# Optimization experiments

Measured on AMD Instinct MI355X. Metric: run time of the kernel, lower is better.

The kernel has to match this reference:

```python
import jax, jax.numpy as jnp
import numpy as np

B, L, E, H, D, DFF = 2, 2048, 1024, 16, 64, 4096
SCALE = D ** 0.5


def rmsnorm(x):
    # NOTE: original uses mean(x*x)**0.5 with no eps and no learned scale
    rms = jnp.sqrt(jnp.mean(x * x, axis=-1, keepdims=True))
    return x / rms


def alibi_matrix():
    i = jnp.arange(L)
    dists = -jnp.abs(i[None, :] - i[:, None]).astype(jnp.float32)  # [L, L]
    slopes = 2.0 ** (-jnp.linspace(1.0, 8.0, H))                   # [H]
    alibi = slopes[:, None, None] * dists                          # [H, L, L]
    causal = jnp.tril(jnp.ones((L, L), dtype=bool))
    return jnp.where(causal[None], alibi, -jnp.inf)[None]          # [1, H, L, L]


def setup_inputs() -> dict:
    key = jax.random.key(0)
    ks = jax.random.split(key, 16)
    s = 0.02
    return {
        "X": jax.random.normal(ks[0], (B, L, E), jnp.float32),
        "encoder_out": jax.random.normal(ks[1], (B, L, E), jnp.float32),
        # self-attention params
        "Wqkv": jax.random.normal(ks[2], (E, 3 * H * D), jnp.float32) * s,
        "bqkv": jnp.zeros((3 * H * D,), jnp.float32),
        "Wo_sa": jax.random.normal(ks[3], (H * D, E), jnp.float32) * s,
        "bo_sa": jnp.zeros((E,), jnp.float32),
        # cross-attention params (computed by torch module but its forward returns X, so unused)
        "Wq": jax.random.normal(ks[4], (E, H * D), jnp.float32) * s,
        "bq": jnp.zeros((H * D,), jnp.float32),
        "Wkv": jax.random.normal(ks[5], (E, 2 * H * D), jnp.float32) * s,
        "bkv": jnp.zeros((2 * H * D,), jnp.float32),
        "Wo_ca": jax.random.normal(ks[6], (H * D, E), jnp.float32) * s,
        "bo_ca": jnp.zeros((E,), jnp.float32),
        # GLU FFN params (bias=False)
        "Ww": jax.random.normal(ks[7], (E, DFF), jnp.float32) * s,
        "Wv": jax.random.normal(ks[8], (E, DFF), jnp.float32) * s,
        "Wout": jax.random.normal(ks[9], (DFF, E), jnp.float32) * s,
    }


def reference(X, encoder_out, Wqkv, bqkv, Wo_sa, bo_sa, Wq, bq, Wkv, bkv,
              Wo_ca, bo_ca, Ww, Wv, Wout):
    alibi = alibi_matrix()

    # ---- self-attention (pre-norm + residual) ----
    h = rmsnorm(X)
    qkv = (h @ Wqkv + bqkv).reshape(B, L, H, 3, D)
    Q, K, V = qkv[..., 0, :], qkv[..., 1, :], qkv[..., 2, :]      # [B, L, H, D]
    scores = jnp.einsum('blhd,bmhd->bhlm', Q, K) / SCALE + alibi  # [B, H, L, L]
    attn = jax.nn.softmax(scores, axis=-1)
    ctx = jnp.einsum('bhlm,bmhd->blhd', attn, V).reshape(B, L, H * D)
    X = X + ctx @ Wo_sa + bo_sa

    # ---- cross-attention stage ----
    # Faithful to source: CrossAttention.forward returns its input X (the
    # normalized tensor) rather than the attention output, so this block is
    # X + rmsnorm(X). Cross-attn params never affect the output.
    X = X + rmsnorm(X)

    # ---- GLU FFN (pre-norm + residual), exact (erf) GELU as in torch F.gelu ----
    h = rmsnorm(X)
    ff = jax.nn.gelu(h @ Ww, approximate=False) * (h @ Wv)
    X = X + ff @ Wout
    return X
```

## Files before the change

### kernel.cpp

```cpp
#include <hip/hip_runtime.h>

#define B_SZ 2
#define L_SEQ 2048
#define E_DIM 1024
#define NH 16
#define DH 64
#define DFF_DIM 4096
#define ROWS (B_SZ * L_SEQ)
#define NCID 80

typedef __attribute__((ext_vector_type(8))) short short8;
typedef __attribute__((ext_vector_type(4))) float f32x4;

__device__ __forceinline__ short f2bf(float f) {
  unsigned u = __builtin_bit_cast(unsigned, f);
  u = (u + 0x7FFFu + ((u >> 16) & 1u)) >> 16;
  return (short)u;
}
__device__ __forceinline__ float bf2f(short s) {
  unsigned u = ((unsigned)(unsigned short)s) << 16;
  return __builtin_bit_cast(float, u);
}
__device__ __forceinline__ unsigned pack2bf(float lo, float hi) {
  return ((unsigned)(unsigned short)f2bf(hi) << 16) |
         (unsigned)(unsigned short)f2bf(lo);
}

__device__ __forceinline__ float fast_gelu(float x) {
  float ax = fabsf(x) * 0.70710678118654752f;
  float t = __builtin_amdgcn_rcpf(__builtin_fmaf(0.3275911f, ax, 1.0f));
  float p = t * __builtin_fmaf(
                    t,
                    __builtin_fmaf(
                        t,
                        __builtin_fmaf(t,
                                       __builtin_fmaf(t, 1.061405429f,
                                                      -1.453152027f),
                                       1.421413741f),
                        -0.284496736f),
                    0.254829592f);
  float erf = 1.0f - p * __expf(-ax * ax);
  erf = copysignf(erf, x);
  return 0.5f * x * (1.0f + erf);
}

__device__ __forceinline__ void async_copy16(const void* g, void* l) {
  __builtin_amdgcn_global_load_lds(
      (const __attribute__((address_space(1))) void*)g,
      (__attribute__((address_space(3))) void*)l, 16, 0, 0);
}

__device__ __forceinline__ float block_sum256(float v) {
  __shared__ float sbuf[4];
#pragma unroll
  for (int off = 32; off > 0; off >>= 1) v += __shfl_xor(v, off, 64);
  int lane = threadIdx.x & 63, w = threadIdx.x >> 6;
  if (lane == 0) sbuf[w] = v;
  __syncthreads();
  return sbuf[0] + sbuf[1] + sbuf[2] + sbuf[3];
}

__global__ __launch_bounds__(256) void prep_all(
    const float* __restrict__ Wqkv, const float* __restrict__ Wo,
    const float* __restrict__ Ww, const float* __restrict__ Wv,
    const float* __restrict__ Wout, const float* __restrict__ X,
    short* __restrict__ Bqkv3, short* __restrict__ WoT,
    short* __restrict__ Bcat, short* __restrict__ WoutT,
    short* __restrict__ H) {
  __shared__ float tile[32][33];
  int b = blockIdx.x;
  if (b < 16384) {
    const float* W;
    short* Wt;
    int K, N, mode, bx, by;
    if (b < 3072) {
      W = Wqkv; Wt = Bqkv3; K = 1024; N = 3072; mode = 1;
      bx = b % 96; by = b / 96;
    } else if (b < 4096) {
      int c = b - 3072;
      W = Wo; Wt = WoT; K = 1024; N = 1024; mode = 1;
      bx = c & 31; by = c >> 5;
    } else if (b < 8192) {
      int c = b - 4096;
      W = Ww; Wt = Bcat; K = 1024; N = 4096; mode = 2;
      bx = c & 127; by = c >> 7;
    } else if (b < 12288) {
      int c = b - 8192;
      W = Wv; Wt = Bcat; K = 1024; N = 4096; mode = 3;
      bx = c & 127; by = c >> 7;
    } else {
      int c = b - 12288;
      W = Wout; Wt = WoutT; K = 4096; N = 1024; mode = 1;
      bx = c & 31; by = c >> 5;
    }
    int n0 = bx * 32, k0 = by * 32;
    int tx = threadIdx.x & 31, ty = threadIdx.x >> 5;
#pragma unroll
    for (int i = 0; i < 4; i++)
      tile[ty + 8 * i][tx] = W[(size_t)(k0 + ty + 8 * i) * N + n0 + tx];
    __syncthreads();
#pragma unroll
    for (int i = 0; i < 4; i++) {
      int n = n0 + ty + 8 * i;
      int orow = (mode == 1)
                     ? n
                     : ((n >> 5) * 64 + (n & 31) + (mode == 3 ? 32 : 0));
      Wt[(size_t)orow * K + k0 + tx] = f2bf(tile[tx][ty + 8 * i]);
    }
  } else {
    size_t row = b - 16384;
    float4 v = ((const float4*)(X + row * E_DIM))[threadIdx.x];
    float ss = v.x * v.x + v.y * v.y + v.z * v.z + v.w * v.w;
    ss = block_sum256(ss);
    float inv = rsqrtf(ss * (1.0f / E_DIM));
    short* h = H + row * E_DIM + (size_t)threadIdx.x * 4;
    h[0] = f2bf(v.x * inv);
    h[1] = f2bf(v.y * inv);
    h[2] = f2bf(v.z * inv);
    h[3] = f2bf(v.w * inv);
  }
}

__global__ __launch_bounds__(256) void resid_rms_fused(
    const float* __restrict__ X, const float* __restrict__ P0,
    const float* __restrict__ P1, const float* __restrict__ bias,
    float* __restrict__ Xout, short* __restrict__ H) {
  size_t row = blockIdx.x;
  int t = threadIdx.x;
  float4 v = ((const float4*)(X + row * E_DIM))[t];
  float4 a = ((const float4*)(P0 + row * E_DIM))[t];
  float4 b = ((const float4*)(P1 + row * E_DIM))[t];
  float4 c = ((const float4*)bias)[t];
  v.x += a.x + b.x + c.x;
  v.y += a.y + b.y + c.y;
  v.z += a.z + b.z + c.z;
  v.w += a.w + b.w + c.w;
  float ss = v.x * v.x + v.y * v.y + v.z * v.z + v.w * v.w;
  ss = block_sum256(ss);
  float inv = rsqrtf(ss * (1.0f / E_DIM));
  float4 o;
  o.x = v.x * (1.0f + inv);
  o.y = v.y * (1.0f + inv);
  o.z = v.z * (1.0f + inv);
  o.w = v.w * (1.0f + inv);
  ((float4*)(Xout + row * E_DIM))[t] = o;
  short* h = H + row * E_DIM + (size_t)t * 4;
  h[0] = f2bf(v.x * inv);
  h[1] = f2bf(v.y * inv);
  h[2] = f2bf(v.z * inv);
  h[3] = f2bf(v.w * inv);
}

__global__ __launch_bounds__(256) void add2_k(const float* __restrict__ P0,
                                              const float* __restrict__ P1,
                                              float* __restrict__ out) {
  size_t i = (size_t)blockIdx.x * 256 + threadIdx.x;
  float4 v = ((const float4*)out)[i];
  float4 a = ((const float4*)P0)[i];
  float4 b = ((const float4*)P1)[i];
  v.x += a.x + b.x;
  v.y += a.y + b.y;
  v.z += a.z + b.z;
  v.w += a.w + b.w;
  ((float4*)out)[i] = v;
}

__global__ __launch_bounds__(256, 2) void gemm_bt(
    const short* __restrict__ A, const short* __restrict__ Bt,
    const float* __restrict__ bias, void* __restrict__ out,
    void* __restrict__ out2, void* __restrict__ out3, int M, int N, int K,
    int epi, int ksplit) {
  __shared__ short smem[128 * 32 * 4];
  short* As0 = smem;
  short* Bs0 = smem + 4096;
  short* As1 = smem + 8192;
  short* Bs1 = smem + 12288;
  int t = threadIdx.x;
  int lane = t & 63;
  int quad = lane >> 4, l16 = lane & 15;
  int wave = t >> 6;
  int wr = wave >> 1, wc = wave & 1;
  int m0 = blockIdx.y * 128, n0 = blockIdx.x * 128;
  int klen = K / ksplit;
  int kstart = blockIdx.z * klen;

  f32x4 acc[4][4];
#pragma unroll
  for (int i = 0; i < 4; i++)
#pragma unroll
    for (int j = 0; j < 4; j++) acc[i][j] = (f32x4){0.f, 0.f, 0.f, 0.f};

  for (int k0 = kstart; k0 < kstart + klen; k0 += 64) {
    __syncthreads();
#pragma unroll
    for (int p = 0; p < 2; p++) {
      int s = p * 256 + t;
      int mm = s >> 2, kk = (s & 3) * 8;
      const short* ag = A + (size_t)(m0 + mm) * K + k0 + kk;
      const short* bg = Bt + (size_t)(n0 + mm) * K + k0 + kk;
      async_copy16(ag, As0 + (size_t)s * 8);
      async_copy16(bg, Bs0 + (size_t)s * 8);
      async_copy16(ag + 32, As1 + (size_t)s * 8);
      async_copy16(bg + 32, Bs1 + (size_t)s * 8);
    }
    __syncthreads();
#pragma unroll
    for (int half = 0; half < 2; half++) {
      const short* As = half ? As1 : As0;
      const short* Bs = half ? Bs1 : Bs0;
      short8 af[4], bfv[4];
#pragma unroll
      for (int i = 0; i < 4; i++) {
        af[i] = *(const short8*)&As[(wr * 64 + i * 16 + l16) * 32 + quad * 8];
        bfv[i] = *(const short8*)&Bs[(wc * 64 + i * 16 + l16) * 32 + quad * 8];
      }
#pragma unroll
      for (int mi = 0; mi < 4; mi++)
#pragma unroll
        for (int ni = 0; ni < 4; ni++)
          acc[mi][ni] = __builtin_amdgcn_mfma_f32_16x16x32_bf16(
              af[mi], bfv[ni], acc[mi][ni], 0, 0, 0);
    }
  }

  if (epi == 5) {
    short* FF = (short*)out;
    int ffbase = blockIdx.x * 64 + wc * 32;
#pragma unroll
    for (int mi = 0; mi < 4; mi++)
#pragma unroll
      for (int ni = 0; ni < 2; ni++)
#pragma unroll
        for (int r = 0; r < 4; r++) {
          int rowl = wr * 64 + mi * 16 + quad * 4 + r;
          float g = fast_gelu(acc[mi][ni][r]);
          FF[(size_t)(m0 + rowl) * DFF_DIM + ffbase + ni * 16 + l16] =
              f2bf(g * acc[mi][ni + 2][r]);
        }
    return;
  }

#pragma unroll
  for (int mi = 0; mi < 4; mi++) {
#pragma unroll
    for (int ni = 0; ni < 4; ni++) {
      int col = n0 + wc * 64 + ni * 16 + l16;
#pragma unroll
      for (int r = 0; r < 4; r++) {
        int row = m0 + wr * 64 + mi * 16 + quad * 4 + r;
        float v = acc[mi][ni][r];
        if (epi == 4) {
          float* po = (float*)out + (size_t)blockIdx.z * ((size_t)M * N);
          po[(size_t)row * N + col] = v;
        } else {
          v += bias[col];
          int h = col / 192;
          int rem = col - h * 192;
          int ty = rem >> 6, d = rem & 63;
          short* dst = (ty == 0) ? (short*)out
                                 : ((ty == 1) ? (short*)out2 : (short*)out3);
          int bb = row >> 11, l = row & 2047;
          dst[((size_t)(bb * NH + h) * L_SEQ + l) * DH + d] = f2bf(v);
        }
      }
    }
  }
}

__global__ __launch_bounds__(512, 2) void gemm256(
    const short* __restrict__ A, const short* __restrict__ Bt,
    const float* __restrict__ bias, void* __restrict__ out,
    void* __restrict__ out2, void* __restrict__ out3, int M, int N, int K,
    int epi) {
  __shared__ __align__(16) short smem[65536];
  (void)M;
  (void)N;
  int t = threadIdx.x;
  int lane = t & 63;
  int quad = lane >> 4, l16 = lane & 15;
  int wave = t >> 6;
  int wr = wave >> 2;
  int wc = wave & 3;
  int m0 = blockIdx.y * 256, n0 = blockIdx.x * 256;

  int row0 = t >> 3;
  int sl = (t & 7) ^ (row0 & 7);
  int goff = row0 * K + sl * 8;
  int ldw = t * 16;
  char* smc = (char*)smem;
  auto stageHT = [&](const short* gsrc, int ldsbase) {
    async_copy16(gsrc + goff, smc + ldsbase + ldw);
    async_copy16(gsrc + goff + (K << 6), smc + ldsbase + 8192 + ldw);
  };

  int swz = (l16 & 7) << 4;
  int colp0 = (quad * 16) ^ swz;
  int colp1 = (64 + quad * 16) ^ swz;
  const char* aB = smc + wr * 16384 + l16 * 128;
  const char* bB = smc + 32768 + (wc >> 1) * 16384 + (wc & 1) * 8192 +
                   l16 * 128;

  f32x4 acc[8][4];
#pragma unroll
  for (int i = 0; i < 8; i++)
#pragma unroll
    for (int j = 0; j < 4; j++) acc[i][j] = (f32x4){0.f, 0.f, 0.f, 0.f};
  short8 areg[4][2], breg[4][2];

  const short* Am0 = A + (size_t)m0 * K;
  const short* Am1 = A + (size_t)(m0 + 128) * K;
  const short* Bn0 = Bt + (size_t)n0 * K;
  const short* Bn1 = Bt + (size_t)(n0 + 128) * K;

  stageHT(Am0, 0);
  stageHT(Am1, 16384);
  stageHT(Bn0, 32768);
  stageHT(Bn1, 49152);
  stageHT(Bn0 + 64, 98304);
  stageHT(Bn1 + 64, 114688);
  asm volatile("s_waitcnt vmcnt(4)" ::: "memory");
  __builtin_amdgcn_s_barrier();

  int NJ = K >> 7;
  for (int j = 0; j < NJ; ++j) {
    int kb = j << 7;
    bool lastI = (j == NJ - 1);
#pragma unroll
    for (int ph = 0; ph < 8; ++ph) {
      const int sub = ph & 3;
      const int mq = sub >> 1;
      const int nq = sub & 1;
      const int dOff = (ph >> 2) ? 65536 : 0;
      if (sub == 0 || sub == 2) {
#pragma unroll
        for (int im = 0; im < 4; ++im) {
          areg[im][0] =
              *(const short8*)(aB + dOff + (mq * 4 + im) * 2048 + colp0);
          areg[im][1] =
              *(const short8*)(aB + dOff + (mq * 4 + im) * 2048 + colp1);
        }
      }
      if (sub <= 1) {
#pragma unroll
        for (int in = 0; in < 2; ++in) {
          breg[nq * 2 + in][0] =
              *(const short8*)(bB + dOff + (nq * 2 + in) * 2048 + colp0);
          breg[nq * 2 + in][1] =
              *(const short8*)(bB + dOff + (nq * 2 + in) * 2048 + colp1);
        }
      }
      if (ph == 0) stageHT(Am0 + kb + 64, 65536);
      if (ph == 1) stageHT(Am1 + kb + 64, 65536 + 16384);
      if (!lastI) {
        if (ph == 2) stageHT(Bn0 + kb + 128, 32768);
        if (ph == 3) stageHT(Bn1 + kb + 128, 49152);
        if (ph == 4) stageHT(Am0 + kb + 128, 0);
        if (ph == 5) stageHT(Am1 + kb + 128, 16384);
        if (ph == 6) stageHT(Bn0 + kb + 192, 98304);
        if (ph == 7) stageHT(Bn1 + kb + 192, 114688);
      }
      __builtin_amdgcn_s_barrier();
      asm volatile("s_waitcnt lgkmcnt(0)" ::: "memory");
      __builtin_amdgcn_sched_barrier(0);
      __builtin_amdgcn_s_setprio(1);
#pragma unroll
      for (int im = 0; im < 4; ++im)
#pragma unroll
        for (int in = 0; in < 2; ++in)
#pragma unroll
          for (int kh = 0; kh < 2; ++kh)
            acc[mq * 4 + im][nq * 2 + in] =
                __builtin_amdgcn_mfma_f32_16x16x32_bf16(
                    areg[im][kh], breg[nq * 2 + in][kh],
                    acc[mq * 4 + im][nq * 2 + in], 0, 0, 0);
      __builtin_amdgcn_s_setprio(0);
      if (ph == 3) {
        if (lastI)
          asm volatile("s_waitcnt vmcnt(0)" ::: "memory");
        else
          asm volatile("s_waitcnt vmcnt(4)" ::: "memory");
      }
      if (ph == 7 && !lastI)
        asm volatile("s_waitcnt vmcnt(4)" ::: "memory");
      __builtin_amdgcn_s_barrier();
    }
  }

  if (epi == 5) {
    short* FF = (short*)out;
    int ffbase = (n0 + wc * 64) >> 1;
#pragma unroll
    for (int mi = 0; mi < 8; ++mi)
#pragma unroll
      for (int ni = 0; ni < 2; ++ni)
#pragma unroll
        for (int r = 0; r < 4; ++r) {
          int rowl = wr * 128 + mi * 16 + quad * 4 + r;
          float g = fast_gelu(acc[mi][ni][r]);
          FF[(size_t)(m0 + rowl) * DFF_DIM + ffbase + ni * 16 + l16] =
              f2bf(g * acc[mi][ni + 2][r]);
        }
    return;
  }
#pragma unroll
  for (int mi = 0; mi < 8; ++mi) {
#pragma unroll
    for (int ni = 0; ni < 4; ++ni) {
      int col = n0 + wc * 64 + ni * 16 + l16;
      float bv = bias[col];
      int h = col / 192;
      int rem = col - h * 192;
      int ty = rem >> 6, d = rem & 63;
      short* dst =
          (ty == 0) ? (short*)out : ((ty == 1) ? (short*)out2 : (short*)out3);
#pragma unroll
      for (int r = 0; r < 4; ++r) {
        int row = m0 + wr * 128 + mi * 16 + quad * 4 + r;
        float v = acc[mi][ni][r] + bv;
        int bb = row >> 11, l = row & 2047;
        dst[((size_t)(bb * NH + h) * L_SEQ + l) * DH + d] = f2bf(v);
      }
    }
  }
}

__global__ __launch_bounds__(256) void v_transp(const short* __restrict__ Vh,
                                                short* __restrict__ VTh) {
  int lt = blockIdx.x, bh = blockIdx.y;
  __shared__ short vtile[64 * 72];
  int t = threadIdx.x;
  int r = t >> 3, c = (t & 7) * 8;
  const short* src = Vh + ((size_t)bh * L_SEQ + lt * 64) * DH;
#pragma unroll
  for (int p = 0; p < 2; p++) {
    int row = r + p * 32;
    short8 vv = *(const short8*)(src + (size_t)row * DH + c);
    *(short8*)&vtile[row * 72 + c] = vv;
  }
  __syncthreads();
#pragma unroll
  for (int p = 0; p < 2; p++) {
    int d = r + p * 32;
    short8 o;
#pragma unroll
    for (int u = 0; u < 8; u++) o[u] = vtile[(c + u) * 72 + d];
    *(short8*)(VTh + ((size_t)bh * DH + d) * L_SEQ + lt * 64 + c) = o;
  }
}

__global__ __launch_bounds__(256) void attn_k(const short* __restrict__ Qh,
                                              const short* __restrict__ Kh,
                                              const short* __restrict__ VTh,
                                              float* __restrict__ OP,
                                              float* __restrict__ RS) {
  int cid = blockIdx.x;
  int bh = blockIdx.y;
  int h = bh & 15;
  int qt, ch;
  if (cid < 8) {
    qt = cid; ch = 0;
  } else if (cid < 24) {
    qt = 8 + ((cid - 8) >> 1); ch = (cid - 8) & 1;
  } else if (cid < 48) {
    qt = 16 + (cid - 24) / 3; ch = (cid - 24) % 3;
  } else {
    qt = 24 + ((cid - 48) >> 2); ch = (cid - 48) & 3;
  }
  int t0 = ch * 8;
  int tend = min(t0 + 8, qt + 1);

  int t = threadIdx.x;
  int wave = t >> 6, lane = t & 63;
  int quad = lane >> 4, l16 = lane & 15;

  __shared__ short kt[128 * 72];
  __shared__ short vt[64 * 136];

  const float L2E = 1.4426950408889634f;
  const float slope = exp2f(-(1.0f + (7.0f / 15.0f) * (float)h));
  const float slopeL = slope * L2E;
  int iw = qt * 64 + wave * 16;

  short8 qf[2];
  {
    const short* qp = Qh + ((size_t)bh * L_SEQ + iw + l16) * DH + quad * 8;
    qf[0] = *(const short8*)(qp);
    qf[1] = *(const short8*)(qp + 32);
  }

  f32x4 o[4];
#pragma unroll
  for (int i = 0; i < 4; i++) o[i] = (f32x4){0.f, 0.f, 0.f, 0.f};
  float rs = 0.f;
  const int irow = iw + l16;
  const float base_l = -slopeL * (float)irow - 8.0f * L2E;

  int sr = t >> 3, sc = (t & 7) * 8;
  const short* kg = Kh + (size_t)bh * L_SEQ * DH;
  const short* vg = VTh + (size_t)bh * DH * L_SEQ;
  short8 kreg[4], vreg[4];
  auto loadKV = [&](int j0) {
    kreg[0] = *(const short8*)(kg + (size_t)(j0 + sr) * DH + sc);
    kreg[1] = *(const short8*)(kg + (size_t)(j0 + sr + 32) * DH + sc);
    kreg[2] = *(const short8*)(kg + (size_t)(j0 + sr + 64) * DH + sc);
    kreg[3] = *(const short8*)(kg + (size_t)(j0 + sr + 96) * DH + sc);
    vreg[0] = *(const short8*)(vg + (size_t)sr * L_SEQ + j0 + sc);
    vreg[1] = *(const short8*)(vg + (size_t)(sr + 32) * L_SEQ + j0 + sc);
    vreg[2] = *(const short8*)(vg + (size_t)sr * L_SEQ + j0 + 64 + sc);
    vreg[3] = *(const short8*)(vg + (size_t)(sr + 32) * L_SEQ + j0 + 64 + sc);
  };
  loadKV(t0 * 64);

  const int sA = l16 + ((quad & 1) << 5);
  const int sB = sA + 16;

  for (int tp = t0; tp < tend; tp += 2) {
    __syncthreads();
    *(short8*)&kt[sr * 72 + sc] = kreg[0];
    *(short8*)&kt[(sr + 32) * 72 + sc] = kreg[1];
    *(short8*)&kt[(sr + 64) * 72 + sc] = kreg[2];
    *(short8*)&kt[(sr + 96) * 72 + sc] = kreg[3];
    *(short8*)&vt[sr * 136 + sc] = vreg[0];
    *(short8*)&vt[(sr + 32) * 136 + sc] = vreg[1];
    *(short8*)&vt[sr * 136 + 64 + sc] = vreg[2];
    *(short8*)&vt[(sr + 32) * 136 + 64 + sc] = vreg[3];
    __syncthreads();
    if (tp + 2 < tend) loadKV((tp + 2) * 64);
    int te = min(tp + 2, tend);
    for (int tix = tp; tix < te; ++tix) {
      int sub = tix - tp;
      int j0 = tix * 64;
      f32x4 s[4];
      __builtin_amdgcn_s_setprio(1);
#pragma unroll
      for (int nt = 0; nt < 4; nt++) {
        f32x4 a = (f32x4){0.f, 0.f, 0.f, 0.f};
#pragma unroll
        for (int ks = 0; ks < 2; ks++) {
          short8 kf = *(const short8*)&kt[(sub * 64 + nt * 16 + l16) * 72 +
                                          ks * 32 + quad * 8];
          a = __builtin_amdgcn_mfma_f32_16x16x32_bf16(kf, qf[ks], a, 0, 0, 0);
        }
        s[nt] = a;
      }
      __builtin_amdgcn_s_setprio(0);
      bool diag = (tix == qt);
      unsigned w[4][2];
#pragma unroll
      for (int nt = 0; nt < 4; nt++) {
        int jb_i = j0 + nt * 16 + quad * 4;
        float jb = __builtin_fmaf(slopeL, (float)jb_i, base_l);
        float pv[4];
#pragma unroll
        for (int r = 0; r < 4; r++) {
          float v = __builtin_fmaf(s[nt][r], 0.18033688011117129f,
                                   jb + slopeL * (float)r);
          if (diag && jb_i + r > irow) v = -1e30f;
          float p = exp2f(v);
          rs += p;
          pv[r] = p;
        }
        w[nt][0] = pack2bf(pv[0], pv[1]);
        w[nt][1] = pack2bf(pv[2], pv[3]);
      }
      bool hiq = (quad & 2) != 0;
      union {
        unsigned u[4];
        short8 v;
      } pk0, pk1;
      {
        unsigned x0 = __shfl((int)w[0][0], sA, 64);
        unsigned y0 = __shfl((int)w[1][0], sA, 64);
        pk0.u[0] = hiq ? y0 : x0;
        unsigned x1 = __shfl((int)w[0][1], sA, 64);
        unsigned y1 = __shfl((int)w[1][1], sA, 64);
        pk0.u[1] = hiq ? y1 : x1;
        unsigned x2 = __shfl((int)w[0][0], sB, 64);
        unsigned y2 = __shfl((int)w[1][0], sB, 64);
        pk0.u[2] = hiq ? y2 : x2;
        unsigned x3 = __shfl((int)w[0][1], sB, 64);
        unsigned y3 = __shfl((int)w[1][1], sB, 64);
        pk0.u[3] = hiq ? y3 : x3;
        unsigned z0 = __shfl((int)w[2][0], sA, 64);
        unsigned q0 = __shfl((int)w[3][0], sA, 64);
        pk1.u[0] = hiq ? q0 : z0;
        unsigned z1 = __shfl((int)w[2][1], sA, 64);
        unsigned q1 = __shfl((int)w[3][1], sA, 64);
        pk1.u[1] = hiq ? q1 : z1;
        unsigned z2 = __shfl((int)w[2][0], sB, 64);
        unsigned q2 = __shfl((int)w[3][0], sB, 64);
        pk1.u[2] = hiq ? q2 : z2;
        unsigned z3 = __shfl((int)w[2][1], sB, 64);
        unsigned q3 = __shfl((int)w[3][1], sB, 64);
        pk1.u[3] = hiq ? q3 : z3;
      }
      __builtin_amdgcn_s_setprio(1);
#pragma unroll
      for (int nt = 0; nt < 4; nt++) {
        short8 bv0 = *(const short8*)&vt[(nt * 16 + l16) * 136 + sub * 64 +
                                         quad * 8];
        o[nt] = __builtin_amdgcn_mfma_f32_16x16x32_bf16(pk0.v, bv0, o[nt], 0,
                                                        0, 0);
        short8 bv1 = *(const short8*)&vt[(nt * 16 + l16) * 136 + sub * 64 +
                                         32 + quad * 8];
        o[nt] = __builtin_amdgcn_mfma_f32_16x16x32_bf16(pk1.v, bv1, o[nt], 0,
                                                        0, 0);
      }
      __builtin_amdgcn_s_setprio(0);
    }
  }
  rs += __shfl_xor(rs, 16, 64);
  rs += __shfl_xor(rs, 32, 64);
  float* op = OP + ((size_t)bh * NCID + cid) * 64 * 64;
  float* rsp = RS + ((size_t)bh * NCID + cid) * 64;
#pragma unroll
  for (int r = 0; r < 4; r++) {
    int rowl = wave * 16 + quad * 4 + r;
#pragma unroll
    for (int nt = 0; nt < 4; nt++) op[rowl * 64 + nt * 16 + l16] = o[nt][r];
  }
  if (quad == 0) rsp[wave * 16 + l16] = rs;
}

__global__ __launch_bounds__(256) void attn_merge(const float* __restrict__ OP,
                                                  const float* __restrict__ RS,
                                                  short* __restrict__ ctx) {
  int row = blockIdx.x;
  int b = row >> 11, i = row & 2047;
  int qt = i >> 6, rowin = i & 63;
  int base, nch;
  if (qt < 8) {
    base = qt; nch = 1;
  } else if (qt < 16) {
    base = 8 + 2 * (qt - 8); nch = 2;
  } else if (qt < 24) {
    base = 24 + 3 * (qt - 16); nch = 3;
  } else {
    base = 48 + 4 * (qt - 24); nch = 4;
  }
  int t = threadIdx.x;
  int col = t * 4;
  int h = col >> 6;
  int bh = b * NH + h;
  float4 o = {0.f, 0.f, 0.f, 0.f};
  float l = 0.f;
  for (int s = 0; s < nch; s++) {
    size_t cb = ((size_t)bh * NCID + base + s) * 64 + rowin;
    float4 v = *(const float4*)&OP[cb * 64 + (col & 63)];
    o.x += v.x;
    o.y += v.y;
    o.z += v.z;
    o.w += v.w;
    l += RS[cb];
  }
  float inv = 1.0f / l;
  short* dst = ctx + (size_t)row * (NH * DH) + col;
  dst[0] = f2bf(o.x * inv);
  dst[1] = f2bf(o.y * inv);
  dst[2] = f2bf(o.z * inv);
  dst[3] = f2bf(o.w * inv);
}

extern "C" void kernel_launch(void* const* d_in, const int* in_sizes, int n_in,
                              void* d_out, int out_size, void* d_ws,
                              size_t ws_size, hipStream_t stream) {
  const float* X = (const float*)d_in[0];
  const float* Wqkv = (const float*)d_in[2];
  const float* bqkv = (const float*)d_in[3];
  const float* Wo_sa = (const float*)d_in[4];
  const float* bo_sa = (const float*)d_in[5];
  const float* Ww = (const float*)d_in[12];
  const float* Wv = (const float*)d_in[13];
  const float* Wout = (const float*)d_in[14];

  char* ws = (char*)d_ws;
  auto take = [&](size_t bytes) {
    char* p = ws;
    ws += (bytes + 255) & ~(size_t)255;
    return p;
  };
  short* Bqkv3 = (short*)take((size_t)3072 * 1024 * 2);
  short* WoT = (short*)take((size_t)E_DIM * E_DIM * 2);
  short* Bcat = (short*)take((size_t)2 * DFF_DIM * E_DIM * 2);
  short* WoutT = (short*)take((size_t)E_DIM * DFF_DIM * 2);
  short* Hbuf = (short*)take((size_t)ROWS * E_DIM * 2);
  short* Qh = (short*)take((size_t)ROWS * NH * DH * 2);
  short* Kh = (short*)take((size_t)ROWS * NH * DH * 2);
  short* Vh = (short*)take((size_t)ROWS * NH * DH * 2);
  short* VTh = (short*)take((size_t)ROWS * NH * DH * 2);
  short* CTX = (short*)take((size_t)ROWS * NH * DH * 2);
  char* big = take((size_t)48 * 1024 * 1024);
  float* OP = (float*)big;
  float* RS = OP + (size_t)B_SZ * NH * NCID * 64 * 64;
  float* Pwo = (float*)(big + (size_t)16 * 1024 * 1024);
  short* FF = (short*)Pwo;
  float* Pwout = (float*)Qh;
  (void)ws_size;
  (void)in_sizes;
  (void)n_in;
  (void)out_size;

  dim3 blk(256);
  prep_all<<<16384 + ROWS, blk, 0, stream>>>(Wqkv, Wo_sa, Ww, Wv, Wout, X,
                                             Bqkv3, WoT, Bcat, WoutT, Hbuf);
  gemm256<<<dim3(3072 / 256, ROWS / 256), dim3(512), 0, stream>>>(
      Hbuf, Bqkv3, bqkv, Qh, Kh, Vh, ROWS, 3072, 1024, 6);
  v_transp<<<dim3(L_SEQ / 64, B_SZ * NH), blk, 0, stream>>>(Vh, VTh);
  attn_k<<<dim3(NCID, B_SZ * NH), blk, 0, stream>>>(Qh, Kh, VTh, OP, RS);
  attn_merge<<<ROWS, blk, 0, stream>>>(OP, RS, CTX);
  gemm_bt<<<dim3(1024 / 128, ROWS / 128, 2), blk, 0, stream>>>(
      CTX, WoT, nullptr, Pwo, nullptr, nullptr, ROWS, 1024, 1024, 4, 2);
  resid_rms_fused<<<ROWS, blk, 0, stream>>>(
      X, Pwo, Pwo + (size_t)ROWS * E_DIM, bo_sa, (float*)d_out, Hbuf);
  gemm256<<<dim3(2 * DFF_DIM / 256, ROWS / 256), dim3(512), 0, stream>>>(
      Hbuf, Bcat, nullptr, FF, nullptr, nullptr, ROWS, 2 * DFF_DIM, 1024, 5);
  gemm_bt<<<dim3(1024 / 128, ROWS / 128, 2), blk, 0, stream>>>(
      FF, WoutT, nullptr, Pwout, nullptr, nullptr, ROWS, 1024, 4096, 4, 2);
  add2_k<<<ROWS * E_DIM / (256 * 4), blk, 0, stream>>>(
      Pwout, Pwout + (size_t)ROWS * E_DIM, (float*)d_out);
}
```

Measured before the change: 408.2 us.

## Drop split-KV attention partitioning and fuse merge normalization into attention epilogue

Each attention block now handles one query tile over its full causal KV range, with heavy tiles scheduled first, and writes normalized bf16 context directly. This removes the separate merge kernel and the fp32 partial-output round trip through global memory. The trade-off is fewer blocks and a longer critical path for the largest tiles, which may hurt load balance across CUs.

```diff
diff --git a/kernel.cpp b/kernel.cpp
--- a/kernel.cpp
+++ b/kernel.cpp
@@ -7,7 +7,6 @@
 #define DH 64
 #define DFF_DIM 4096
 #define ROWS (B_SZ * L_SEQ)
-#define NCID 80
 
 typedef __attribute__((ext_vector_type(8))) short short8;
 typedef __attribute__((ext_vector_type(4))) float f32x4;
@@ -451,23 +450,11 @@
 __global__ __launch_bounds__(256) void attn_k(const short* __restrict__ Qh,
                                               const short* __restrict__ Kh,
                                               const short* __restrict__ VTh,
-                                              float* __restrict__ OP,
-                                              float* __restrict__ RS) {
-  int cid = blockIdx.x;
+                                              short* __restrict__ CTX) {
+  int qt = 31 - blockIdx.x;
   int bh = blockIdx.y;
-  int h = bh & 15;
-  int qt, ch;
-  if (cid < 8) {
-    qt = cid; ch = 0;
-  } else if (cid < 24) {
-    qt = 8 + ((cid - 8) >> 1); ch = (cid - 8) & 1;
-  } else if (cid < 48) {
-    qt = 16 + (cid - 24) / 3; ch = (cid - 24) % 3;
-  } else {
-    qt = 24 + ((cid - 48) >> 2); ch = (cid - 48) & 3;
-  }
-  int t0 = ch * 8;
-  int tend = min(t0 + 8, qt + 1);
+  int b = bh >> 4, h = bh & 15;
+  int tend = qt + 1;
 
   int t = threadIdx.x;
   int wave = t >> 6, lane = t & 63;
@@ -509,12 +496,12 @@
     vreg[2] = *(const short8*)(vg + (size_t)sr * L_SEQ + j0 + 64 + sc);
     vreg[3] = *(const short8*)(vg + (size_t)(sr + 32) * L_SEQ + j0 + 64 + sc);
   };
-  loadKV(t0 * 64);
+  loadKV(0);
 
   const int sA = l16 + ((quad & 1) << 5);
   const int sB = sA + 16;
 
-  for (int tp = t0; tp < tend; tp += 2) {
+  for (int tp = 0; tp < tend; tp += 2) {
     __syncthreads();
     *(short8*)&kt[sr * 72 + sc] = kreg[0];
     *(short8*)&kt[(sr + 32) * 72 + sc] = kreg[1];
@@ -611,54 +598,16 @@
   }
   rs += __shfl_xor(rs, 16, 64);
   rs += __shfl_xor(rs, 32, 64);
-  float* op = OP + ((size_t)bh * NCID + cid) * 64 * 64;
-  float* rsp = RS + ((size_t)bh * NCID + cid) * 64;
 #pragma unroll
   for (int r = 0; r < 4; r++) {
-    int rowl = wave * 16 + quad * 4 + r;
-#pragma unroll
-    for (int nt = 0; nt < 4; nt++) op[rowl * 64 + nt * 16 + l16] = o[nt][r];
-  }
-  if (quad == 0) rsp[wave * 16 + l16] = rs;
-}
-
-__global__ __launch_bounds__(256) void attn_merge(const float* __restrict__ OP,
-                                                  const float* __restrict__ RS,
-                                                  short* __restrict__ ctx) {
-  int row = blockIdx.x;
-  int b = row >> 11, i = row & 2047;
-  int qt = i >> 6, rowin = i & 63;
-  int base, nch;
-  if (qt < 8) {
-    base = qt; nch = 1;
-  } else if (qt < 16) {
-    base = 8 + 2 * (qt - 8); nch = 2;
-  } else if (qt < 24) {
-    base = 24 + 3 * (qt - 16); nch = 3;
-  } else {
-    base = 48 + 4 * (qt - 24); nch = 4;
-  }
-  int t = threadIdx.x;
-  int col = t * 4;
-  int h = col >> 6;
-  int bh = b * NH + h;
-  float4 o = {0.f, 0.f, 0.f, 0.f};
-  float l = 0.f;
-  for (int s = 0; s < nch; s++) {
-    size_t cb = ((size_t)bh * NCID + base + s) * 64 + rowin;
-    float4 v = *(const float4*)&OP[cb * 64 + (col & 63)];
-    o.x += v.x;
-    o.y += v.y;
-    o.z += v.z;
-    o.w += v.w;
-    l += RS[cb];
-  }
-  float inv = 1.0f / l;
-  short* dst = ctx + (size_t)row * (NH * DH) + col;
-  dst[0] = f2bf(o.x * inv);
-  dst[1] = f2bf(o.y * inv);
-  dst[2] = f2bf(o.z * inv);
-  dst[3] = f2bf(o.w * inv);
+    float rsr = __shfl(rs, quad * 4 + r, 64);
+    float inv = 1.0f / rsr;
+    int l = iw + quad * 4 + r;
+    short* dp = CTX + ((size_t)(b * L_SEQ + l)) * (NH * DH) + h * DH;
+#pragma unroll
+    for (int nt = 0; nt < 4; nt++)
+      dp[nt * 16 + l16] = f2bf(o[nt][r] * inv);
+  }
 }
 
 extern "C" void kernel_launch(void* const* d_in, const int* in_sizes, int n_in,
@@ -690,8 +639,6 @@
   short* VTh = (short*)take((size_t)ROWS * NH * DH * 2);
   short* CTX = (short*)take((size_t)ROWS * NH * DH * 2);
   char* big = take((size_t)48 * 1024 * 1024);
-  float* OP = (float*)big;
-  float* RS = OP + (size_t)B_SZ * NH * NCID * 64 * 64;
   float* Pwo = (float*)(big + (size_t)16 * 1024 * 1024);
   short* FF = (short*)Pwo;
   float* Pwout = (float*)Qh;
@@ -706,8 +653,7 @@
   gemm256<<<dim3(3072 / 256, ROWS / 256), dim3(512), 0, stream>>>(
       Hbuf, Bqkv3, bqkv, Qh, Kh, Vh, ROWS, 3072, 1024, 6);
   v_transp<<<dim3(L_SEQ / 64, B_SZ * NH), blk, 0, stream>>>(Vh, VTh);
-  attn_k<<<dim3(NCID, B_SZ * NH), blk, 0, stream>>>(Qh, Kh, VTh, OP, RS);
-  attn_merge<<<ROWS, blk, 0, stream>>>(OP, RS, CTX);
+  attn_k<<<dim3(32, B_SZ * NH), blk, 0, stream>>>(Qh, Kh, VTh, CTX);
   gemm_bt<<<dim3(1024 / 128, ROWS / 128, 2), blk, 0, stream>>>(
       CTX, WoT, nullptr, Pwo, nullptr, nullptr, ROWS, 1024, 1024, 4, 2);
   resid_rms_fused<<<ROWS, blk, 0, stream>>>(
```

Result: slower. 427.5 us (+4.7%).
